# Kernel optimization log

Measured on AMD Instinct MI355X. Metric: run time of the kernel, lower is better.

## Reference

```python
import math
import jax, jax.numpy as jnp
import numpy as np

N0 = N1 = 100000
E = 200000
IN = OUT = 128
H = 8
DK = OUT // H
T = 2
R = 3


def setup_inputs() -> dict:
    key = jax.random.key(0)
    ks = jax.random.split(key, 24)
    s = 1.0 / math.sqrt(IN)
    inp = {
        'h0': jax.random.normal(ks[0], (N0, IN), jnp.float32),
        'h1': jax.random.normal(ks[1], (N1, IN), jnp.float32),
        'kw': jax.random.normal(ks[2], (T, IN, OUT), jnp.float32) * s,
        'kb': jax.random.normal(ks[3], (T, OUT), jnp.float32) * 0.01,
        'qw': jax.random.normal(ks[4], (T, IN, OUT), jnp.float32) * s,
        'qb': jax.random.normal(ks[5], (T, OUT), jnp.float32) * 0.01,
        'vw': jax.random.normal(ks[6], (T, IN, OUT), jnp.float32) * s,
        'vb': jax.random.normal(ks[7], (T, OUT), jnp.float32) * 0.01,
        'aw': jax.random.normal(ks[8], (T, OUT, OUT), jnp.float32) * (1.0 / math.sqrt(OUT)),
        'ab': jax.random.normal(ks[9], (T, OUT), jnp.float32) * 0.01,
        'rel_att': jax.random.normal(ks[10], (R, H, DK, DK), jnp.float32) * (1.0 / math.sqrt(DK)),
        'rel_msg': jax.random.normal(ks[11], (R, H, DK, DK), jnp.float32) * (1.0 / math.sqrt(DK)),
        'rel_pri': jnp.ones((R, H), jnp.float32),
        'skip': jnp.ones((T,), jnp.float32),
        'src0': jax.random.randint(ks[12], (E,), 0, N1, jnp.int32),  # author -> paper
        'dst0': jax.random.randint(ks[13], (E,), 0, N0, jnp.int32),
        'src1': jax.random.randint(ks[14], (E,), 0, N0, jnp.int32),  # paper -> author
        'dst1': jax.random.randint(ks[15], (E,), 0, N1, jnp.int32),
        'src2': jax.random.randint(ks[16], (E,), 0, N0, jnp.int32),  # paper -> paper
        'dst2': jax.random.randint(ks[17], (E,), 0, N0, jnp.int32),
    }
    return inp


def _edge_softmax(score, dst, n_dst):
    # segment softmax normalized by destination node (norm_by='dst')
    m = jax.ops.segment_max(score, dst, num_segments=n_dst)
    e = jnp.exp(score - m[dst])
    s = jax.ops.segment_sum(e, dst, num_segments=n_dst)
    return e / s[dst]


def reference(h0, h1, kw, kb, qw, qb, vw, vb, aw, ab, rel_att, rel_msg,
              rel_pri, skip, src0, dst0, src1, dst1, src2, dst2):
    n_heads, d_k = rel_att.shape[1], rel_att.shape[2]
    sqrt_dk = math.sqrt(d_k)
    hs = (h0, h1)
    Ns = (h0.shape[0], h1.shape[0])
    # per-type K/Q/V projections, reshaped to [N, H, d_k]
    k = [(hs[t] @ kw[t] + kb[t]).reshape(-1, n_heads, d_k) for t in range(2)]
    q = [(hs[t] @ qw[t] + qb[t]).reshape(-1, n_heads, d_k) for t in range(2)]
    v = [(hs[t] @ vw[t] + vb[t]).reshape(-1, n_heads, d_k) for t in range(2)]
    # (relation id, src node type, dst node type, src idx, dst idx)
    rels = ((0, 1, 0, src0, dst0), (1, 0, 1, src1, dst1), (2, 0, 0, src2, dst2))
    agg = {0: [], 1: []}
    for r, st, dt, s_idx, d_idx in rels:
        kk = jnp.einsum('nij,ijk->nik', k[st], rel_att[r])
        vv = jnp.einsum('nij,ijk->nik', v[st], rel_msg[r])
        score = (q[dt][d_idx] * kk[s_idx]).sum(-1) * rel_pri[r] / sqrt_dk  # [E,H]
        attn = _edge_softmax(score, d_idx, Ns[dt])
        msg = vv[s_idx] * attn[..., None]  # [E,H,d_k]
        agg[dt].append(jax.ops.segment_sum(msg, d_idx, num_segments=Ns[dt]))
    outs = []
    for t in range(2):
        tt = sum(agg[t]) / len(agg[t])  # cross_reducer='mean'
        tt = tt.reshape(Ns[t], n_heads * d_k)
        trans = tt @ aw[t] + ab[t]  # dropout in eval mode -> identity
        alpha = jax.nn.sigmoid(skip[t])
        outs.append(trans * alpha + hs[t] * (1.0 - alpha))
    return jnp.stack(outs)  # [2, N, out_dim] (N0 == N1)
```

## Files before the change

kernel.cpp:

```cpp
#include <hip/hip_runtime.h>
#include <stdint.h>

typedef __attribute__((ext_vector_type(8))) short s16x8;
typedef __attribute__((ext_vector_type(4))) float f32x4;

__device__ __forceinline__ ushort f2bf(float x) {
  union { float f; uint32_t u; } v; v.f = x;
  uint32_t r = v.u + 0x7FFFu + ((v.u >> 16) & 1u);
  return (ushort)(r >> 16);
}
__device__ __forceinline__ float bf2f(ushort u) {
  union { uint32_t u; float f; } v; v.u = ((uint32_t)u) << 16; return v.f;
}

__device__ __forceinline__ void barrier_lds_only() {
  asm volatile("s_waitcnt lgkmcnt(0)" ::: "memory");
  __builtin_amdgcn_s_barrier();
}

__global__ __launch_bounds__(256) void prep_weights(
    const float* __restrict__ kw, const float* __restrict__ kb,
    const float* __restrict__ qw, const float* __restrict__ qb,
    const float* __restrict__ vw, const float* __restrict__ vb,
    const float* __restrict__ aw, const float* __restrict__ ab,
    const float* __restrict__ rel_att, const float* __restrict__ rel_msg,
    ushort* __restrict__ WT, float* __restrict__ BIAS)
{
  int slot = blockIdx.x, tid = threadIdx.x;
  const float* W; const float* b; const float* rel = nullptr; int mode;
  switch (slot) {
    case 0: W = kw;         b = kb;       mode = 0; break;
    case 1: W = kw + 16384; b = kb + 128; mode = 0; break;
    case 2: W = vw;         b = vb;       mode = 0; break;
    case 3: W = vw + 16384; b = vb + 128; mode = 0; break;
    case 4: W = qw;         b = qb;       rel = rel_att;        mode = 1; break;
    case 5: W = qw + 16384; b = qb + 128; rel = rel_att + 2048; mode = 1; break;
    case 6: W = qw;         b = qb;       rel = rel_att + 4096; mode = 1; break;
    case 7: W = aw;         b = ab;       rel = rel_msg;        mode = 2; break;
    case 8: W = aw + 16384; b = ab + 128; rel = rel_msg + 2048; mode = 2; break;
    default: W = aw;        b = ab;       rel = rel_msg + 4096; mode = 2; break;
  }
  ushort* out = WT + slot * 16384;
  for (int e = tid; e < 16384; e += 256) {
    int c = e >> 7, k = e & 127;
    float val;
    if (mode == 0) {
      val = W[k*128 + c];
    } else if (mode == 1) {
      int h = c >> 4, cc = c & 15;
      float s = 0.f;
      #pragma unroll
      for (int j = 0; j < 16; j++) s += W[k*128 + h*16 + j] * rel[h*256 + cc*16 + j];
      val = s;
    } else {
      int hr = k >> 4, ir = k & 15;
      float s = 0.f;
      #pragma unroll
      for (int j = 0; j < 16; j++) s += rel[hr*256 + ir*16 + j] * W[(hr*16 + j)*128 + c];
      val = s;
    }
    out[c*128 + k] = f2bf(val);
  }
  if (tid < 128) {
    int c = tid; float val;
    if (mode == 1) {
      int h = c >> 4, cc = c & 15;
      float s = 0.f;
      #pragma unroll
      for (int j = 0; j < 16; j++) s += b[h*16 + j] * rel[h*256 + cc*16 + j];
      val = s;
    } else {
      val = b[c];
    }
    BIAS[slot*128 + c] = val;
  }
}

__global__ __launch_bounds__(256) void proj_fused(
    const float* __restrict__ h0, const float* __restrict__ h1,
    const ushort* __restrict__ WT, const float* __restrict__ BIAS,
    ushort* __restrict__ P, int N)
{
  __shared__ ushort ALDS0[64 * 132];
  __shared__ ushort ALDS1[64 * 132];

  int src_t = blockIdx.y;
  const float* A = src_t ? h1 : h0;
  int nslots = src_t ? 3 : 4;
  unsigned smap = src_t ? 0x531u : 0x6420u;

  int tid = threadIdx.x;
  int lane = tid & 63;
  int wave = tid >> 6;
  int lr = lane & 15, lh = lane >> 4;
  int colbase = (wave & 1) * 64;
  int rowhalf = wave >> 1;

  int base = blockIdx.x * 64;
  if (base >= N) return;

  s16x8 af[2][4];
  #pragma unroll
  for (int rg = 0; rg < 2; rg++) {
    int arow = base + rowhalf*32 + rg*16 + lr;
    if (arow >= N) arow = N - 1;
    #pragma unroll
    for (int ks = 0; ks < 4; ks++) {
      const float* ap = A + (size_t)arow*128 + ks*32 + lh*8;
      f32x4 x0 = *(const f32x4*)ap;
      f32x4 x1 = *(const f32x4*)(ap + 4);
      s16x8 v;
      #pragma unroll
      for (int j = 0; j < 4; j++) { v[j] = (short)f2bf(x0[j]); v[4+j] = (short)f2bf(x1[j]); }
      af[rg][ks] = v;
    }
  }

  auto compute_slot = [&](int g, ushort* L) {
    const ushort* Bt = WT + g * 16384;
    const float* bias = BIAS + g * 128;
    #pragma unroll
    for (int ct = 0; ct < 4; ct++) {
      int col = colbase + ct*16 + lr;
      s16x8 bfr[4];
      #pragma unroll
      for (int ks = 0; ks < 4; ks++)
        bfr[ks] = *(const s16x8*)(Bt + col*128 + ks*32 + lh*8);
      float bb = bias[col];
      #pragma unroll
      for (int rg = 0; rg < 2; rg++) {
        f32x4 acc = { bb, bb, bb, bb };
        #pragma unroll
        for (int ks = 0; ks < 4; ks++)
          acc = __builtin_amdgcn_mfma_f32_16x16x32_bf16(af[rg][ks], bfr[ks], acc, 0, 0, 0);
        int rl0 = rowhalf*32 + rg*16 + lh*4;
        #pragma unroll
        for (int i = 0; i < 4; i++)
          L[(rl0 + i) * 132 + col] = f2bf(acc[i]);
      }
    }
  };

  auto copyout = [&](int g, const ushort* L) {
    ushort* C = P + (size_t)g * N * 128;
    #pragma unroll
    for (int j = 0; j < 4; j++) {
      int idx = j * 256 + tid;
      int row = idx >> 4, ch = idx & 15;
      int gr = base + row;
      if (gr < N)
        __builtin_nontemporal_store(
            *(const s16x8*)(L + row * 132 + ch * 8),
            (s16x8*)(C + (size_t)gr * 128 + ch * 8));
    }
  };

  int prev = smap & 15;
  compute_slot(prev, ALDS0);
  barrier_lds_only();
  for (int si = 1; si < nslots; si++) {
    int g = (smap >> (si * 4)) & 15;
    ushort* cur = (si & 1) ? ALDS1 : ALDS0;
    const ushort* pv = (si & 1) ? ALDS0 : ALDS1;
    copyout(prev, pv);
    compute_slot(g, cur);
    barrier_lds_only();
    prev = g;
  }
  copyout(prev, (nslots & 1) ? ALDS0 : ALDS1);
}

__global__ void count_edges(const int* __restrict__ d0, const int* __restrict__ d1,
                            const int* __restrict__ d2, int* __restrict__ counts,
                            int E, int N)
{
  int idx = blockIdx.x * 256 + threadIdx.x;
  if (idx >= 3 * E) return;
  int r = idx / E, e = idx - r * E;
  const int* D = (r == 0) ? d0 : (r == 1) ? d1 : d2;
  atomicAdd(counts + r * N + D[e], 1);
}

#define SCAN_CHUNK 2048
#define MAXC 1024

__global__ __launch_bounds__(256) void scan_partial(
    const int* __restrict__ counts, int* __restrict__ offsets,
    int* __restrict__ bsum, int N)
{
  int r = blockIdx.y, c = blockIdx.x, tid = threadIdx.x;
  const int* cnt = counts + (size_t)r * N;
  int* o = offsets + (size_t)r * (N + 1);
  int idx0 = c * SCAN_CHUNK + tid * 8;
  int p[8]; int run = 0;
  #pragma unroll
  for (int j = 0; j < 8; j++) {
    int v = (idx0 + j < N) ? cnt[idx0 + j] : 0;
    run += v; p[j] = run;
  }
  int lane = tid & 63, wid = tid >> 6;
  int x = run;
  #pragma unroll
  for (int off = 1; off < 64; off <<= 1) {
    int t = __shfl_up(x, off, 64);
    if (lane >= off) x += t;
  }
  __shared__ int wsum[4];
  if (lane == 63) wsum[wid] = x;
  __syncthreads();
  int woff = 0;
  for (int wph = 0; wph < wid; wph++) woff += wsum[wph];
  int texcl = woff + x - run;
  #pragma unroll
  for (int j = 0; j < 8; j++)
    if (idx0 + j < N) o[idx0 + j + 1] = texcl + p[j];
  if (tid == 255) bsum[r * MAXC + c] = woff + x;
}

__global__ void scan_bsums(int* __restrict__ bsum, int nchunks)
{
  int r = blockIdx.x, lane = threadIdx.x;
  int carry = 0;
  for (int base = 0; base < nchunks; base += 64) {
    int i = base + lane;
    int v0 = (i < nchunks) ? bsum[r * MAXC + i] : 0;
    int x = v0;
    #pragma unroll
    for (int off = 1; off < 64; off <<= 1) {
      int t = __shfl_up(x, off, 64);
      if (lane >= off) x += t;
    }
    if (i < nchunks) bsum[r * MAXC + i] = carry + x - v0;
    carry += __shfl(x, 63, 64);
  }
}

__global__ __launch_bounds__(256) void scan_add(
    int* __restrict__ offsets, const int* __restrict__ bsum, int N)
{
  int r = blockIdx.y, c = blockIdx.x, tid = threadIdx.x;
  int* o = offsets + (size_t)r * (N + 1);
  if (c == 0 && tid == 0) o[0] = 0;
  int add = bsum[r * MAXC + c];
  if (add == 0) return;
  int idx0 = c * SCAN_CHUNK + tid * 8;
  #pragma unroll
  for (int j = 0; j < 8; j++) {
    int i = idx0 + j;
    if (i < N) o[i + 1] += add;
  }
}

__global__ void scatter_edges(const int* __restrict__ d0, const int* __restrict__ d1,
                              const int* __restrict__ d2,
                              const int* __restrict__ s0, const int* __restrict__ s1,
                              const int* __restrict__ s2,
                              const int* __restrict__ offsets, int* __restrict__ cursor,
                              int* __restrict__ slist, int E, int N)
{
  int idx = blockIdx.x * 256 + threadIdx.x;
  if (idx >= 3 * E) return;
  int r = idx / E, e = idx - r * E;
  const int* D = (r == 0) ? d0 : (r == 1) ? d1 : d2;
  const int* S = (r == 0) ? s0 : (r == 1) ? s1 : s2;
  int dst = D[e];
  int pos = offsets[r * (N + 1) + dst] + atomicAdd(cursor + r * N + dst, 1);
  slist[r * E + pos] = S[e];
}

__global__ __launch_bounds__(256) void agg_final(
    const int* __restrict__ slist, const int* __restrict__ offs,
    const ushort* __restrict__ P,
    const ushort* __restrict__ WT, const float* __restrict__ BIAS,
    const float* __restrict__ h0, const float* __restrict__ h1,
    const float* __restrict__ rel_pri, const float* __restrict__ skip,
    float* __restrict__ out, int N, int E)
{
  __shared__ ushort T0[32 * 132];
  __shared__ ushort T1[32 * 132];

  int ty = blockIdx.y;
  int tid = threadIdx.x;
  int dstl = tid >> 3, h = tid & 7;
  int base = blockIdx.x * 32;
  int dst = base + dstl;
  bool valid = dst < N;
  const float* H = ty ? h1 : h0;
  float* outT = out + (size_t)ty * N * 128;

  const ushort* K0 = P;
  const ushort* K1 = P + (size_t)1 * N * 128;
  const ushort* V0 = P + (size_t)2 * N * 128;
  const ushort* V1 = P + (size_t)3 * N * 128;

  {
    int rA = ty ? 1 : 0;
    const int* sl = slist + (size_t)rA * E;
    const int* of = offs + (size_t)rA * (N + 1);
    const ushort* K = ty ? K0 : K1;
    const ushort* V = ty ? V0 : V1;
    const ushort* QT = P + (size_t)(ty ? 5 : 4) * N * 128;

    float qf[16];
    const ushort* qr = QT + (size_t)(valid ? dst : 0) * 128 + h * 16;
    #pragma unroll
    for (int j = 0; j < 16; j++) qf[j] = bf2f(qr[j]);
    float pr = rel_pri[rA * 8 + h] * 0.25f;

    float acc[16];
    #pragma unroll
    for (int j = 0; j < 16; j++) acc[j] = 0.f;
    float sum = 0.f;
    int b0 = valid ? of[dst] : 0, b1 = valid ? of[dst + 1] : 0;
    if (b1 > b0) {
      int scur = sl[b0];
      const ushort* kr = K + (size_t)scur * 128 + h * 16;
      const ushort* vr = V + (size_t)scur * 128 + h * 16;
      s16x8 k0 = *(const s16x8*)kr, k1 = *(const s16x8*)(kr + 8);
      s16x8 v0 = *(const s16x8*)vr, v1 = *(const s16x8*)(vr + 8);
      for (int i = b0; i < b1; i++) {
        int snx = (i + 1 < b1) ? sl[i + 1] : scur;
        const ushort* krn = K + (size_t)snx * 128 + h * 16;
        const ushort* vrn = V + (size_t)snx * 128 + h * 16;
        s16x8 k0n = *(const s16x8*)krn, k1n = *(const s16x8*)(krn + 8);
        s16x8 v0n = *(const s16x8*)vrn, v1n = *(const s16x8*)(vrn + 8);
        float sc = 0.f;
        #pragma unroll
        for (int j = 0; j < 8; j++)
          sc += qf[j] * bf2f((ushort)k0[j]) + qf[8+j] * bf2f((ushort)k1[j]);
        float w = __expf(sc * pr);
        #pragma unroll
        for (int j = 0; j < 8; j++) {
          acc[j]   += w * bf2f((ushort)v0[j]);
          acc[8+j] += w * bf2f((ushort)v1[j]);
        }
        sum += w;
        k0 = k0n; k1 = k1n; v0 = v0n; v1 = v1n;
      }
    }
    float inv = (b1 > b0) ? 1.0f / sum : 0.f;
    ushort* a0 = T0 + dstl * 132 + h * 16;
    #pragma unroll
    for (int j = 0; j < 16; j++) a0[j] = f2bf(acc[j] * inv);
  }

  if (ty == 0) {
    const int* sl = slist + (size_t)2 * E;
    const int* of = offs + (size_t)2 * (N + 1);
    const ushort* K = K0;
    const ushort* V = V0;
    const ushort* QT = P + (size_t)6 * N * 128;

    float qf[16];
    const ushort* qr = QT + (size_t)(valid ? dst : 0) * 128 + h * 16;
    #pragma unroll
    for (int j = 0; j < 16; j++) qf[j] = bf2f(qr[j]);
    float pr = rel_pri[2 * 8 + h] * 0.25f;

    float acc[16];
    #pragma unroll
    for (int j = 0; j < 16; j++) acc[j] = 0.f;
    float sum = 0.f;
    int b0 = valid ? of[dst] : 0, b1 = valid ? of[dst + 1] : 0;
    if (b1 > b0) {
      int scur = sl[b0];
      const ushort* kr = K + (size_t)scur * 128 + h * 16;
      const ushort* vr = V + (size_t)scur * 128 + h * 16;
      s16x8 k0 = *(const s16x8*)kr, k1 = *(const s16x8*)(kr + 8);
      s16x8 v0 = *(const s16x8*)vr, v1 = *(const s16x8*)(vr + 8);
      for (int i = b0; i < b1; i++) {
        int snx = (i + 1 < b1) ? sl[i + 1] : scur;
        const ushort* krn = K + (size_t)snx * 128 + h * 16;
        const ushort* vrn = V + (size_t)snx * 128 + h * 16;
        s16x8 k0n = *(const s16x8*)krn, k1n = *(const s16x8*)(krn + 8);
        s16x8 v0n = *(const s16x8*)vrn, v1n = *(const s16x8*)(vrn + 8);
        float sc = 0.f;
        #pragma unroll
        for (int j = 0; j < 8; j++)
          sc += qf[j] * bf2f((ushort)k0[j]) + qf[8+j] * bf2f((ushort)k1[j]);
        float w = __expf(sc * pr);
        #pragma unroll
        for (int j = 0; j < 8; j++) {
          acc[j]   += w * bf2f((ushort)v0[j]);
          acc[8+j] += w * bf2f((ushort)v1[j]);
        }
        sum += w;
        k0 = k0n; k1 = k1n; v0 = v0n; v1 = v1n;
      }
    }
    float inv = (b1 > b0) ? 1.0f / sum : 0.f;
    ushort* a1 = T1 + dstl * 132 + h * 16;
    #pragma unroll
    for (int j = 0; j < 16; j++) a1[j] = f2bf(acc[j] * inv);
  }
  __syncthreads();

  int lane = tid & 63, wv = tid >> 6;
  int lr = lane & 15, lh = lane >> 4;
  int rowhalf = wv & 1, colhalf = wv >> 1;
  int fA = ty ? 8 : 7;
  const float* bias = BIAS + fA * 128;
  float alpha = 1.0f / (1.0f + __expf(-skip[ty]));
  float beta = 1.0f - alpha;
  float rscale = ty ? 1.0f : 0.5f;

  s16x8 afA[4], afB[4];
  int arow_l = rowhalf * 16 + lr;
  #pragma unroll
  for (int ks = 0; ks < 4; ks++)
    afA[ks] = *(const s16x8*)(T0 + arow_l * 132 + ks * 32 + lh * 8);
  if (ty == 0) {
    #pragma unroll
    for (int ks = 0; ks < 4; ks++)
      afB[ks] = *(const s16x8*)(T1 + arow_l * 132 + ks * 32 + lh * 8);
  }

  #pragma unroll
  for (int ct = 0; ct < 4; ct++) {
    int col = colhalf * 64 + ct * 16 + lr;
    const ushort* BtA = WT + fA * 16384;
    s16x8 bfrA[4];
    #pragma unroll
    for (int ks = 0; ks < 4; ks++)
      bfrA[ks] = *(const s16x8*)(BtA + col * 128 + ks * 32 + lh * 8);
    f32x4 acc = { 0.f, 0.f, 0.f, 0.f };
    #pragma unroll
    for (int ks = 0; ks < 4; ks++)
      acc = __builtin_amdgcn_mfma_f32_16x16x32_bf16(afA[ks], bfrA[ks], acc, 0, 0, 0);
    if (ty == 0) {
      const ushort* BtB = WT + 9 * 16384;
      s16x8 bfrB[4];
      #pragma unroll
      for (int ks = 0; ks < 4; ks++)
        bfrB[ks] = *(const s16x8*)(BtB + col * 128 + ks * 32 + lh * 8);
      #pragma unroll
      for (int ks = 0; ks < 4; ks++)
        acc = __builtin_amdgcn_mfma_f32_16x16x32_bf16(afB[ks], bfrB[ks], acc, 0, 0, 0);
    }
    float bb = bias[col];
    int r0l = rowhalf * 16 + lh * 4;
    #pragma unroll
    for (int i = 0; i < 4; i++) {
      int g = base + r0l + i;
      if (g < N) {
        size_t off = (size_t)g * 128 + col;
        __builtin_nontemporal_store((acc[i] * rscale + bb) * alpha + H[off] * beta,
                                    &outT[off]);
      }
    }
  }
}

extern "C" void kernel_launch(void* const* d_in, const int* in_sizes, int n_in,
                              void* d_out, int out_size, void* d_ws, size_t ws_size,
                              hipStream_t stream)
{
  const float* h0      = (const float*)d_in[0];
  const float* h1      = (const float*)d_in[1];
  const float* kw      = (const float*)d_in[2];
  const float* kb      = (const float*)d_in[3];
  const float* qw      = (const float*)d_in[4];
  const float* qb      = (const float*)d_in[5];
  const float* vw      = (const float*)d_in[6];
  const float* vb      = (const float*)d_in[7];
  const float* aw      = (const float*)d_in[8];
  const float* ab      = (const float*)d_in[9];
  const float* rel_att = (const float*)d_in[10];
  const float* rel_msg = (const float*)d_in[11];
  const float* rel_pri = (const float*)d_in[12];
  const float* skip    = (const float*)d_in[13];
  const int* s0 = (const int*)d_in[14];
  const int* d0 = (const int*)d_in[15];
  const int* s1 = (const int*)d_in[16];
  const int* d1 = (const int*)d_in[17];
  const int* s2 = (const int*)d_in[18];
  const int* d2 = (const int*)d_in[19];

  int N = in_sizes[0] / 128;
  int E = in_sizes[14];

  char* w = (char*)d_ws;
  size_t o = 0;
  auto alloc = [&](size_t bytes) { size_t cur = o; o += (bytes + 255) / 256 * 256; return cur; };
  ushort* WT   = (ushort*)(w + alloc((size_t)10 * 16384 * 2));
  float*  BIAS = (float*) (w + alloc((size_t)10 * 128 * 4));
  ushort* P    = (ushort*)(w + alloc((size_t)7 * N * 128 * 2));
  int* counts  = (int*)   (w + alloc((size_t)3 * N * 4));
  int* cursor  = (int*)   (w + alloc((size_t)3 * N * 4));
  int* offs    = (int*)   (w + alloc((size_t)3 * (N + 1) * 4));
  int* slist   = (int*)   (w + alloc((size_t)3 * E * 4));
  int* bsum    = (int*)   (w + alloc((size_t)3 * MAXC * 4));
  (void)ws_size; (void)n_in; (void)out_size;

  hipMemsetAsync(counts, 0, (size_t)3 * N * 4, stream);
  hipMemsetAsync(cursor, 0, (size_t)3 * N * 4, stream);

  prep_weights<<<10, 256, 0, stream>>>(kw, kb, qw, qb, vw, vb, aw, ab,
                                       rel_att, rel_msg, WT, BIAS);

  proj_fused<<<dim3((N + 63) / 64, 2), 256, 0, stream>>>(h0, h1, WT, BIAS, P, N);

  int egrid = (3 * E + 255) / 256;
  count_edges<<<egrid, 256, 0, stream>>>(d0, d1, d2, counts, E, N);

  int nchunks = (N + SCAN_CHUNK - 1) / SCAN_CHUNK;
  scan_partial<<<dim3(nchunks, 3), 256, 0, stream>>>(counts, offs, bsum, N);
  scan_bsums<<<3, 64, 0, stream>>>(bsum, nchunks);
  scan_add<<<dim3(nchunks, 3), 256, 0, stream>>>(offs, bsum, N);

  scatter_edges<<<egrid, 256, 0, stream>>>(d0, d1, d2, s0, s1, s2,
                                           offs, cursor, slist, E, N);

  int fgrid = (N + 31) / 32;
  agg_final<<<dim3(fgrid, 2), 256, 0, stream>>>(
      slist, offs, P, WT, BIAS, h0, h1, rel_pri, skip,
      (float*)d_out, N, E);
}
```

Before: 360.1 us.

## Compute Q projections inside aggregation kernel instead of materializing them

The projection kernel now computes only the K and V slots. The destination-side Q projections are computed per 32-row tile with MFMA directly in the aggregation kernel and staged in LDS. This removes writing and re-reading three N×128 bf16 Q tensors through global memory and shrinks the workspace. In exchange, the aggregation kernel re-reads h rows and Q weights, and gains extra MFMA work and barriers before the edge loop.

```diff
diff --git a/kernel.cpp b/kernel.cpp
--- a/kernel.cpp
+++ b/kernel.cpp
@@ -86,8 +86,8 @@
 
   int src_t = blockIdx.y;
   const float* A = src_t ? h1 : h0;
-  int nslots = src_t ? 3 : 4;
-  unsigned smap = src_t ? 0x531u : 0x6420u;
+  unsigned smap = src_t ? 0x31u : 0x20u;
+  const int nslots = 2;
 
   int tid = threadIdx.x;
   int lane = tid & 63;
@@ -160,14 +160,12 @@
   barrier_lds_only();
   for (int si = 1; si < nslots; si++) {
     int g = (smap >> (si * 4)) & 15;
-    ushort* cur = (si & 1) ? ALDS1 : ALDS0;
-    const ushort* pv = (si & 1) ? ALDS0 : ALDS1;
-    copyout(prev, pv);
-    compute_slot(g, cur);
+    copyout(prev, ALDS0);
+    compute_slot(g, ALDS1);
     barrier_lds_only();
     prev = g;
   }
-  copyout(prev, (nslots & 1) ? ALDS0 : ALDS1);
+  copyout(prev, ALDS1);
 }
 
 __global__ void count_edges(const int* __restrict__ d0, const int* __restrict__ d1,
@@ -293,16 +291,77 @@
   const ushort* V0 = P + (size_t)2 * N * 128;
   const ushort* V1 = P + (size_t)3 * N * 128;
 
+  int lane = tid & 63, wv = tid >> 6;
+  int lr = lane & 15, lh = lane >> 4;
+  int rowhalf = wv & 1, colhalf = wv >> 1;
+
+  {
+    s16x8 af[4];
+    int arow = base + rowhalf*16 + lr;
+    if (arow >= N) arow = N - 1;
+    #pragma unroll
+    for (int ks = 0; ks < 4; ks++) {
+      const float* ap = H + (size_t)arow*128 + ks*32 + lh*8;
+      f32x4 x0 = *(const f32x4*)ap;
+      f32x4 x1 = *(const f32x4*)(ap + 4);
+      s16x8 v;
+      #pragma unroll
+      for (int j = 0; j < 4; j++) { v[j] = (short)f2bf(x0[j]); v[4+j] = (short)f2bf(x1[j]); }
+      af[ks] = v;
+    }
+    int qslotA = ty ? 5 : 4;
+    {
+      const ushort* Bt = WT + qslotA * 16384;
+      const float* bq = BIAS + qslotA * 128;
+      #pragma unroll
+      for (int ct = 0; ct < 4; ct++) {
+        int col = colhalf*64 + ct*16 + lr;
+        s16x8 bfr[4];
+        #pragma unroll
+        for (int ks = 0; ks < 4; ks++)
+          bfr[ks] = *(const s16x8*)(Bt + col*128 + ks*32 + lh*8);
+        float bb = bq[col];
+        f32x4 acc = { bb, bb, bb, bb };
+        #pragma unroll
+        for (int ks = 0; ks < 4; ks++)
+          acc = __builtin_amdgcn_mfma_f32_16x16x32_bf16(af[ks], bfr[ks], acc, 0, 0, 0);
+        int r0l = rowhalf*16 + lh*4;
+        #pragma unroll
+        for (int i = 0; i < 4; i++) T0[(r0l + i)*132 + col] = f2bf(acc[i]);
+      }
+    }
+    if (ty == 0) {
+      const ushort* Bt = WT + 6 * 16384;
+      const float* bq = BIAS + 6 * 128;
+      #pragma unroll
+      for (int ct = 0; ct < 4; ct++) {
+        int col = colhalf*64 + ct*16 + lr;
+        s16x8 bfr[4];
+        #pragma unroll
+        for (int ks = 0; ks < 4; ks++)
+          bfr[ks] = *(const s16x8*)(Bt + col*128 + ks*32 + lh*8);
+        float bb = bq[col];
+        f32x4 acc = { bb, bb, bb, bb };
+        #pragma unroll
+        for (int ks = 0; ks < 4; ks++)
+          acc = __builtin_amdgcn_mfma_f32_16x16x32_bf16(af[ks], bfr[ks], acc, 0, 0, 0);
+        int r0l = rowhalf*16 + lh*4;
+        #pragma unroll
+        for (int i = 0; i < 4; i++) T1[(r0l + i)*132 + col] = f2bf(acc[i]);
+      }
+    }
+  }
+  __syncthreads();
+
   {
     int rA = ty ? 1 : 0;
     const int* sl = slist + (size_t)rA * E;
     const int* of = offs + (size_t)rA * (N + 1);
     const ushort* K = ty ? K0 : K1;
     const ushort* V = ty ? V0 : V1;
-    const ushort* QT = P + (size_t)(ty ? 5 : 4) * N * 128;
 
     float qf[16];
-    const ushort* qr = QT + (size_t)(valid ? dst : 0) * 128 + h * 16;
+    const ushort* qr = T0 + dstl * 132 + h * 16;
     #pragma unroll
     for (int j = 0; j < 16; j++) qf[j] = bf2f(qr[j]);
     float pr = rel_pri[rA * 8 + h] * 0.25f;
@@ -339,6 +398,7 @@
       }
     }
     float inv = (b1 > b0) ? 1.0f / sum : 0.f;
+    __syncthreads();
     ushort* a0 = T0 + dstl * 132 + h * 16;
     #pragma unroll
     for (int j = 0; j < 16; j++) a0[j] = f2bf(acc[j] * inv);
@@ -347,12 +407,9 @@
   if (ty == 0) {
     const int* sl = slist + (size_t)2 * E;
     const int* of = offs + (size_t)2 * (N + 1);
-    const ushort* K = K0;
-    const ushort* V = V0;
-    const ushort* QT = P + (size_t)6 * N * 128;
 
     float qf[16];
-    const ushort* qr = QT + (size_t)(valid ? dst : 0) * 128 + h * 16;
+    const ushort* qr = T1 + dstl * 132 + h * 16;
     #pragma unroll
     for (int j = 0; j < 16; j++) qf[j] = bf2f(qr[j]);
     float pr = rel_pri[2 * 8 + h] * 0.25f;
@@ -364,14 +421,14 @@
     int b0 = valid ? of[dst] : 0, b1 = valid ? of[dst + 1] : 0;
     if (b1 > b0) {
       int scur = sl[b0];
-      const ushort* kr = K + (size_t)scur * 128 + h * 16;
-      const ushort* vr = V + (size_t)scur * 128 + h * 16;
+      const ushort* kr = K0 + (size_t)scur * 128 + h * 16;
+      const ushort* vr = V0 + (size_t)scur * 128 + h * 16;
       s16x8 k0 = *(const s16x8*)kr, k1 = *(const s16x8*)(kr + 8);
       s16x8 v0 = *(const s16x8*)vr, v1 = *(const s16x8*)(vr + 8);
       for (int i = b0; i < b1; i++) {
         int snx = (i + 1 < b1) ? sl[i + 1] : scur;
-        const ushort* krn = K + (size_t)snx * 128 + h * 16;
-        const ushort* vrn = V + (size_t)snx * 128 + h * 16;
+        const ushort* krn = K0 + (size_t)snx * 128 + h * 16;
+        const ushort* vrn = V0 + (size_t)snx * 128 + h * 16;
         s16x8 k0n = *(const s16x8*)krn, k1n = *(const s16x8*)(krn + 8);
         s16x8 v0n = *(const s16x8*)vrn, v1n = *(const s16x8*)(vrn + 8);
         float sc = 0.f;
@@ -389,15 +446,15 @@
       }
     }
     float inv = (b1 > b0) ? 1.0f / sum : 0.f;
+    __syncthreads();
     ushort* a1 = T1 + dstl * 132 + h * 16;
     #pragma unroll
     for (int j = 0; j < 16; j++) a1[j] = f2bf(acc[j] * inv);
+  } else {
+    __syncthreads();
   }
   __syncthreads();
 
-  int lane = tid & 63, wv = tid >> 6;
-  int lr = lane & 15, lh = lane >> 4;
-  int rowhalf = wv & 1, colhalf = wv >> 1;
   int fA = ty ? 8 : 7;
   const float* bias = BIAS + fA * 128;
   float alpha = 1.0f / (1.0f + __expf(-skip[ty]));
@@ -484,7 +541,7 @@
   auto alloc = [&](size_t bytes) { size_t cur = o; o += (bytes + 255) / 256 * 256; return cur; };
   ushort* WT   = (ushort*)(w + alloc((size_t)10 * 16384 * 2));
   float*  BIAS = (float*) (w + alloc((size_t)10 * 128 * 4));
-  ushort* P    = (ushort*)(w + alloc((size_t)7 * N * 128 * 2));
+  ushort* P    = (ushort*)(w + alloc((size_t)4 * N * 128 * 2));
   int* counts  = (int*)   (w + alloc((size_t)3 * N * 4));
   int* cursor  = (int*)   (w + alloc((size_t)3 * N * 4));
   int* offs    = (int*)   (w + alloc((size_t)3 * (N + 1) * 4));
```

New measurement: 399.9 us. 11.1% more time.

## Parallelize edge aggregation over edges with LDS atomics instead of per-destination loops

Applied to the files above, without the earlier changes.

The aggregation phase now assigns edges within each 32-destination tile round-robin to thread groups, instead of having each thread walk its own destination's edge list. Per-destination accumulators move to shared memory and are updated with float atomics, and a new dlist array recording each edge's destination is written during scatter. This targets load imbalance from the Poisson-distributed in-degrees. In exchange it adds 17 LDS atomics per edge per head, reloads Q per edge, costs extra global traffic for dlist, and drops the software prefetch of the next K/V rows.

```diff
diff --git a/kernel.cpp b/kernel.cpp
--- a/kernel.cpp
+++ b/kernel.cpp
@@ -256,7 +256,8 @@
                               const int* __restrict__ s0, const int* __restrict__ s1,
                               const int* __restrict__ s2,
                               const int* __restrict__ offsets, int* __restrict__ cursor,
-                              int* __restrict__ slist, int E, int N)
+                              int* __restrict__ slist, int* __restrict__ dlist,
+                              int E, int N)
 {
   int idx = blockIdx.x * 256 + threadIdx.x;
   if (idx >= 3 * E) return;
@@ -266,25 +267,27 @@
   int dst = D[e];
   int pos = offsets[r * (N + 1) + dst] + atomicAdd(cursor + r * N + dst, 1);
   slist[r * E + pos] = S[e];
+  dlist[r * E + pos] = dst;
 }
 
 __global__ __launch_bounds__(256) void agg_final(
-    const int* __restrict__ slist, const int* __restrict__ offs,
+    const int* __restrict__ slist, const int* __restrict__ dlist,
+    const int* __restrict__ offs,
     const ushort* __restrict__ P,
     const ushort* __restrict__ WT, const float* __restrict__ BIAS,
     const float* __restrict__ h0, const float* __restrict__ h1,
     const float* __restrict__ rel_pri, const float* __restrict__ skip,
     float* __restrict__ out, int N, int E)
 {
+  __shared__ float ACC[32 * 8 * 17];
   __shared__ ushort T0[32 * 132];
   __shared__ ushort T1[32 * 132];
 
   int ty = blockIdx.y;
   int tid = threadIdx.x;
-  int dstl = tid >> 3, h = tid & 7;
+  int grp = tid >> 3, h = tid & 7;
   int base = blockIdx.x * 32;
-  int dst = base + dstl;
-  bool valid = dst < N;
+  int dend = (base + 32 < N) ? base + 32 : N;
   const float* H = ty ? h1 : h0;
   float* outT = out + (size_t)ty * N * 128;
 
@@ -293,107 +296,56 @@
   const ushort* V0 = P + (size_t)2 * N * 128;
   const ushort* V1 = P + (size_t)3 * N * 128;
 
-  {
-    int rA = ty ? 1 : 0;
-    const int* sl = slist + (size_t)rA * E;
-    const int* of = offs + (size_t)rA * (N + 1);
-    const ushort* K = ty ? K0 : K1;
-    const ushort* V = ty ? V0 : V1;
-    const ushort* QT = P + (size_t)(ty ? 5 : 4) * N * 128;
-
-    float qf[16];
-    const ushort* qr = QT + (size_t)(valid ? dst : 0) * 128 + h * 16;
-    #pragma unroll
-    for (int j = 0; j < 16; j++) qf[j] = bf2f(qr[j]);
-    float pr = rel_pri[rA * 8 + h] * 0.25f;
-
-    float acc[16];
-    #pragma unroll
-    for (int j = 0; j < 16; j++) acc[j] = 0.f;
-    float sum = 0.f;
-    int b0 = valid ? of[dst] : 0, b1 = valid ? of[dst + 1] : 0;
-    if (b1 > b0) {
-      int scur = sl[b0];
-      const ushort* kr = K + (size_t)scur * 128 + h * 16;
-      const ushort* vr = V + (size_t)scur * 128 + h * 16;
+  int npass = ty ? 1 : 2;
+  for (int pass = 0; pass < npass; ++pass) {
+    int r = ty ? 1 : (pass ? 2 : 0);
+    const ushort* K = (r == 0) ? K1 : K0;
+    const ushort* V = (r == 0) ? V1 : V0;
+    const ushort* QT = P + (size_t)(4 + r) * N * 128;
+    float pr = rel_pri[r * 8 + h] * 0.25f;
+
+    float* mine = ACC + (grp * 8 + h) * 17;
+    #pragma unroll
+    for (int j = 0; j < 17; j++) mine[j] = 0.f;
+    __syncthreads();
+
+    const int* sl = slist + (size_t)r * E;
+    const int* dl = dlist + (size_t)r * E;
+    int e0 = offs[(size_t)r * (N + 1) + base];
+    int e1 = offs[(size_t)r * (N + 1) + dend];
+    for (int i = e0 + grp; i < e1; i += 32) {
+      int s = sl[i];
+      int d = dl[i] - base;
+      const ushort* qr = QT + (size_t)(base + d) * 128 + h * 16;
+      const ushort* kr = K + (size_t)s * 128 + h * 16;
+      const ushort* vr = V + (size_t)s * 128 + h * 16;
+      s16x8 q0 = *(const s16x8*)qr, q1 = *(const s16x8*)(qr + 8);
       s16x8 k0 = *(const s16x8*)kr, k1 = *(const s16x8*)(kr + 8);
       s16x8 v0 = *(const s16x8*)vr, v1 = *(const s16x8*)(vr + 8);
-      for (int i = b0; i < b1; i++) {
-        int snx = (i + 1 < b1) ? sl[i + 1] : scur;
-        const ushort* krn = K + (size_t)snx * 128 + h * 16;
-        const ushort* vrn = V + (size_t)snx * 128 + h * 16;
-        s16x8 k0n = *(const s16x8*)krn, k1n = *(const s16x8*)(krn + 8);
-        s16x8 v0n = *(const s16x8*)vrn, v1n = *(const s16x8*)(vrn + 8);
-        float sc = 0.f;
-        #pragma unroll
-        for (int j = 0; j < 8; j++)
-          sc += qf[j] * bf2f((ushort)k0[j]) + qf[8+j] * bf2f((ushort)k1[j]);
-        float w = __expf(sc * pr);
-        #pragma unroll
-        for (int j = 0; j < 8; j++) {
-          acc[j]   += w * bf2f((ushort)v0[j]);
-          acc[8+j] += w * bf2f((ushort)v1[j]);
-        }
-        sum += w;
-        k0 = k0n; k1 = k1n; v0 = v0n; v1 = v1n;
+      float sc = 0.f;
+      #pragma unroll
+      for (int j = 0; j < 8; j++)
+        sc += bf2f((ushort)q0[j]) * bf2f((ushort)k0[j])
+            + bf2f((ushort)q1[j]) * bf2f((ushort)k1[j]);
+      float w = __expf(sc * pr);
+      float* a = ACC + (d * 8 + h) * 17;
+      atomicAdd(a + 16, w);
+      #pragma unroll
+      for (int j = 0; j < 8; j++) {
+        atomicAdd(a + j,     w * bf2f((ushort)v0[j]));
+        atomicAdd(a + 8 + j, w * bf2f((ushort)v1[j]));
       }
     }
-    float inv = (b1 > b0) ? 1.0f / sum : 0.f;
-    ushort* a0 = T0 + dstl * 132 + h * 16;
-    #pragma unroll
-    for (int j = 0; j < 16; j++) a0[j] = f2bf(acc[j] * inv);
-  }
-
-  if (ty == 0) {
-    const int* sl = slist + (size_t)2 * E;
-    const int* of = offs + (size_t)2 * (N + 1);
-    const ushort* K = K0;
-    const ushort* V = V0;
-    const ushort* QT = P + (size_t)6 * N * 128;
-
-    float qf[16];
-    const ushort* qr = QT + (size_t)(valid ? dst : 0) * 128 + h * 16;
-    #pragma unroll
-    for (int j = 0; j < 16; j++) qf[j] = bf2f(qr[j]);
-    float pr = rel_pri[2 * 8 + h] * 0.25f;
-
-    float acc[16];
-    #pragma unroll
-    for (int j = 0; j < 16; j++) acc[j] = 0.f;
-    float sum = 0.f;
-    int b0 = valid ? of[dst] : 0, b1 = valid ? of[dst + 1] : 0;
-    if (b1 > b0) {
-      int scur = sl[b0];
-      const ushort* kr = K + (size_t)scur * 128 + h * 16;
-      const ushort* vr = V + (size_t)scur * 128 + h * 16;
-      s16x8 k0 = *(const s16x8*)kr, k1 = *(const s16x8*)(kr + 8);
-      s16x8 v0 = *(const s16x8*)vr, v1 = *(const s16x8*)(vr + 8);
-      for (int i = b0; i < b1; i++) {
-        int snx = (i + 1 < b1) ? sl[i + 1] : scur;
-        const ushort* krn = K + (size_t)snx * 128 + h * 16;
-        const ushort* vrn = V + (size_t)snx * 128 + h * 16;
-        s16x8 k0n = *(const s16x8*)krn, k1n = *(const s16x8*)(krn + 8);
-        s16x8 v0n = *(const s16x8*)vrn, v1n = *(const s16x8*)(vrn + 8);
-        float sc = 0.f;
-        #pragma unroll
-        for (int j = 0; j < 8; j++)
-          sc += qf[j] * bf2f((ushort)k0[j]) + qf[8+j] * bf2f((ushort)k1[j]);
-        float w = __expf(sc * pr);
-        #pragma unroll
-        for (int j = 0; j < 8; j++) {
-          acc[j]   += w * bf2f((ushort)v0[j]);
-          acc[8+j] += w * bf2f((ushort)v1[j]);
-        }
-        sum += w;
-        k0 = k0n; k1 = k1n; v0 = v0n; v1 = v1n;
-      }
-    }
-    float inv = (b1 > b0) ? 1.0f / sum : 0.f;
-    ushort* a1 = T1 + dstl * 132 + h * 16;
-    #pragma unroll
-    for (int j = 0; j < 16; j++) a1[j] = f2bf(acc[j] * inv);
-  }
-  __syncthreads();
+    __syncthreads();
+    {
+      float sum = mine[16];
+      float inv = (sum > 0.f) ? 1.0f / sum : 0.f;
+      ushort* Trow = (pass ? T1 : T0) + grp * 132 + h * 16;
+      #pragma unroll
+      for (int j = 0; j < 16; j++) Trow[j] = f2bf(mine[j] * inv);
+    }
+    __syncthreads();
+  }
 
   int lane = tid & 63, wv = tid >> 6;
   int lr = lane & 15, lh = lane >> 4;
@@ -489,6 +441,7 @@
   int* cursor  = (int*)   (w + alloc((size_t)3 * N * 4));
   int* offs    = (int*)   (w + alloc((size_t)3 * (N + 1) * 4));
   int* slist   = (int*)   (w + alloc((size_t)3 * E * 4));
+  int* dlist   = (int*)   (w + alloc((size_t)3 * E * 4));
   int* bsum    = (int*)   (w + alloc((size_t)3 * MAXC * 4));
   (void)ws_size; (void)n_in; (void)out_size;
 
@@ -509,10 +462,10 @@
   scan_add<<<dim3(nchunks, 3), 256, 0, stream>>>(offs, bsum, N);
 
   scatter_edges<<<egrid, 256, 0, stream>>>(d0, d1, d2, s0, s1, s2,
-                                           offs, cursor, slist, E, N);
+                                           offs, cursor, slist, dlist, E, N);
 
   int fgrid = (N + 31) / 32;
   agg_final<<<dim3(fgrid, 2), 256, 0, stream>>>(
-      slist, offs, P, WT, BIAS, h0, h1, rel_pri, skip,
+      slist, dlist, offs, P, WT, BIAS, h0, h1, rel_pri, skip,
       (float*)d_out, N, E);
 }
```

Measured after the change: 678.4 us. 88.4% more time.
